# Kernel tuning notes

Measured on AMD Instinct MI355X. Metric: run time of the kernel, lower is better.

## Reference

```python
import jax, jax.numpy as jnp
import numpy as np

# Mamba2 defaults (mamba-ssm): expand=2, d_state=128, d_conv=4, headdim=64, ngroups=1
D_MODEL = 1024
D_INNER = 2 * D_MODEL            # 2048
D_STATE = 128
D_CONV = 4
HEADDIM = 64
NHEADS = D_INNER // HEADDIM      # 32
CONV_DIM = D_INNER + 2 * D_STATE # 2304 (x, B, C go through conv)
D_IN_PROJ = 2 * D_INNER + 2 * D_STATE + NHEADS  # 4384 (z, xBC, dt)
LN_EPS = 1e-6


def setup_inputs() -> dict:
    key = jax.random.key(0)
    ks = jax.random.split(key, 12)
    B, L, D = 8, 1024, D_MODEL
    x = jax.random.normal(ks[0], (B, L, D), jnp.float32)
    t = jax.random.normal(ks[1], (B, D), jnp.float32)
    y = jax.random.normal(ks[2], (B, L, D), jnp.float32)
    # adaLN linear (zero-init in the module; use small random values for a non-trivial baseline)
    w_ada = jax.random.normal(ks[3], (D, 3 * D), jnp.float32) * 0.02
    b_ada = jax.random.normal(ks[4], (3 * D,), jnp.float32) * 0.02
    # Mamba2 params
    w_in = jax.random.normal(ks[5], (D, D_IN_PROJ), jnp.float32) * (D ** -0.5)
    conv_w = jax.random.normal(ks[6], (CONV_DIM, D_CONV), jnp.float32) * (D_CONV ** -0.5)
    conv_b = jnp.zeros((CONV_DIM,), jnp.float32)
    # dt_bias = softplus^{-1}(dt) with dt log-uniform in [1e-3, 1e-1]
    dt0 = jnp.exp(jax.random.uniform(ks[7], (NHEADS,)) * (np.log(0.1) - np.log(0.001)) + np.log(0.001))
    dt_bias = dt0 + jnp.log(-jnp.expm1(-dt0))
    A_log = jnp.log(jax.random.uniform(ks[8], (NHEADS,), minval=1.0, maxval=16.0))
    D_param = jnp.ones((NHEADS,), jnp.float32)
    w_out = jax.random.normal(ks[9], (D_INNER, D), jnp.float32) * (D_INNER ** -0.5)
    return {"x": x, "t": t, "y": y, "w_ada": w_ada, "b_ada": b_ada, "w_in": w_in,
            "conv_w": conv_w, "conv_b": conv_b, "dt_bias": dt_bias, "A_log": A_log,
            "D_param": D_param, "w_out": w_out}


def _layernorm(x):
    mu = jnp.mean(x, axis=-1, keepdims=True)
    var = jnp.mean(jnp.square(x - mu), axis=-1, keepdims=True)
    return (x - mu) / jnp.sqrt(var + LN_EPS)


def _mamba2(u, w_in, conv_w, conv_b, dt_bias, A_log, D_param, w_out):
    B, L, _ = u.shape
    zxbcdt = u @ w_in  # [B, L, D_IN_PROJ]
    z = zxbcdt[..., :D_INNER]
    xBC = zxbcdt[..., D_INNER:D_INNER + CONV_DIM]
    dt = zxbcdt[..., D_INNER + CONV_DIM:]
    # depthwise causal conv1d (kernel=4) + silu
    xp = jnp.pad(xBC, ((0, 0), (D_CONV - 1, 0), (0, 0)))
    conv = conv_b
    for k in range(D_CONV):
        conv = conv + conv_w[:, k] * xp[:, k:k + L, :]
    xBC = jax.nn.silu(conv)
    xh = xBC[..., :D_INNER].reshape(B, L, NHEADS, HEADDIM)
    Bm = xBC[..., D_INNER:D_INNER + D_STATE]  # [B, L, N] (ngroups=1)
    Cm = xBC[..., D_INNER + D_STATE:]         # [B, L, N]
    dt = jax.nn.softplus(dt + dt_bias)        # [B, L, H]
    A = -jnp.exp(A_log)                       # [H]
    dA = jnp.exp(dt * A)                      # [B, L, H]
    dtx = dt[..., None] * xh                  # [B, L, H, P]

    def step(h, inp):
        dA_t, dtx_t, B_t, C_t = inp
        # h: [B, H, P, N]
        h = h * dA_t[:, :, None, None] + dtx_t[..., None] * B_t[:, None, None, :]
        y_t = jnp.einsum('bhpn,bn->bhp', h, C_t)
        return h, y_t

    h0 = jnp.zeros((B, NHEADS, HEADDIM, D_STATE), u.dtype)
    xs = (jnp.moveaxis(dA, 1, 0), jnp.moveaxis(dtx, 1, 0),
          jnp.moveaxis(Bm, 1, 0), jnp.moveaxis(Cm, 1, 0))
    _, ys = jax.lax.scan(step, h0, xs)        # ys: [L, B, H, P]
    yv = jnp.moveaxis(ys, 0, 1) + D_param[None, None, :, None] * xh
    yv = yv.reshape(B, L, D_INNER) * jax.nn.silu(z)  # rmsnorm=False -> silu(z) gating
    return yv @ w_out


def reference(x, t, y, w_ada, b_ada, w_in, conv_w, conv_b, dt_bias, A_log, D_param, w_out):
    at = jax.nn.silu(t) @ w_ada + b_ada   # [B, 3D]
    ay = jax.nn.silu(y) @ w_ada + b_ada   # [B, L, 3D]
    sh_t, sc_t, g_t = jnp.split(at, 3, axis=1)
    sh_y, sc_y, g_y = jnp.split(ay, 3, axis=2)
    shift = sh_t[:, None, :] + sh_y
    scale = sc_t[:, None, :] + sc_y
    gate = g_t[:, None, :] + g_y
    mod = _layernorm(x) * (1 + scale) + shift
    return gate * _mamba2(mod, w_in, conv_w, conv_b, dt_bias, A_log, D_param, w_out) + x
```

## Files before the change

kernel.cpp:

```cpp
#include <hip/hip_runtime.h>

typedef float f32x4 __attribute__((ext_vector_type(4)));
typedef __bf16 bf16x8 __attribute__((ext_vector_type(8)));
typedef unsigned short ushort;
typedef ushort ushort8 __attribute__((ext_vector_type(8)));
typedef ushort ushort4v __attribute__((ext_vector_type(4)));

#define DM 1024
#define DI 2048
#define DSTATE 128
#define NH 32
#define HD 64
#define CONVDIM 2304
#define DPROJ 4384
#define ROWS 8192

__device__ __forceinline__ float bf2f(ushort u){
  union { unsigned int i; float f; } v; v.i = ((unsigned int)u)<<16; return v.f;
}
__device__ __forceinline__ ushort f2bf(float f){
  union { float f; unsigned int i; } v; v.f = f;
  unsigned int r = v.i + 0x7FFFu + ((v.i>>16)&1u);
  return (ushort)(r>>16);
}
__device__ __forceinline__ float siluf(float x){ return x / (1.f + __expf(-x)); }

__device__ __forceinline__ void gload16(const ushort* g, ushort* l){
  __builtin_amdgcn_global_load_lds(
      (const __attribute__((address_space(1))) void*)g,
      (__attribute__((address_space(3))) void*)l, 16, 0, 0);
}

__global__ __launch_bounds__(256) void k_silu_cast(const float* __restrict__ in,
                                                   ushort* __restrict__ out, int n){
  int i = (blockIdx.x*256 + threadIdx.x)*4;
  if (i >= n) return;
  float4 v = *(const float4*)(in + i);
  ushort4v o;
  o.x = f2bf(siluf(v.x)); o.y = f2bf(siluf(v.y));
  o.z = f2bf(siluf(v.z)); o.w = f2bf(siluf(v.w));
  *(ushort4v*)(out + i) = o;
}

__global__ __launch_bounds__(256) void k_transpose_cast(const float* __restrict__ in,
                                                        ushort* __restrict__ out,
                                                        int K, int N){
  __shared__ float tile[32][33];
  int n0 = blockIdx.x*32, k0 = blockIdx.y*32;
  int tx = threadIdx.x & 31, ty = threadIdx.x >> 5;
  for (int r = ty; r < 32; r += 8) tile[r][tx] = in[(size_t)(k0+r)*N + n0+tx];
  __syncthreads();
  for (int r = ty; r < 32; r += 8) out[(size_t)(n0+r)*K + k0+tx] = f2bf(tile[tx][r]);
}

__global__ __launch_bounds__(256) void k_at(const float* __restrict__ t,
                                            const float* __restrict__ w_ada,
                                            const float* __restrict__ b_ada,
                                            float* __restrict__ at){
  __shared__ float st[1024];
  int b = blockIdx.y;
  int col = blockIdx.x*256 + threadIdx.x;
  for (int i = threadIdx.x; i < 1024; i += 256) st[i] = siluf(t[b*1024 + i]);
  __syncthreads();
  float acc = 0.f;
  for (int k = 0; k < 1024; ++k) acc += st[k] * w_ada[(size_t)k*3072 + col];
  at[b*3072 + col] = acc + b_ada[col];
}

#define STG(Q, KT) do{ \
  gload16(pA0 + (size_t)(KT)*32, &sm[(Q)*12288 + (wave*2+0)*512]); \
  gload16(pA1 + (size_t)(KT)*32, &sm[(Q)*12288 + (wave*2+1)*512]); \
  gload16(pB0 + (size_t)(KT)*32, &sm[(Q)*12288 + 8192 + wave*512]); }while(0)

#define CMP(BOFF) do{ \
  bf16x8 af[4], bfr[4]; \
  _Pragma("unroll") \
  for (int m=0;m<4;m++) af[m]  = *(const bf16x8*)&sm[(BOFF) + (wr*64 + m*16 + l16)*32 + kbs]; \
  _Pragma("unroll") \
  for (int n=0;n<4;n++) bfr[n] = *(const bf16x8*)&sm[(BOFF) + 8192 + (wc*64 + n*16 + l16)*32 + kbs]; \
  __builtin_amdgcn_s_setprio(1); \
  _Pragma("unroll") \
  for (int m=0;m<4;m++) \
    _Pragma("unroll") \
    for (int n=0;n<4;n++) \
      acc[m][n] = __builtin_amdgcn_mfma_f32_16x16x32_bf16(af[m], bfr[n], acc[m][n], 0, 0, 0); \
  __builtin_amdgcn_s_setprio(0); }while(0)

#define BODY(Q, T) do{ \
  STG(((Q)+2)%3, (T)+2); \
  CMP((Q)*12288); \
  asm volatile("s_waitcnt vmcnt(3)" ::: "memory"); \
  __builtin_amdgcn_s_barrier(); \
  __builtin_amdgcn_sched_barrier(0); }while(0)

template<int EPI>
__global__ __launch_bounds__(512)
void k_gemm(const ushort* __restrict__ Ag, const ushort* __restrict__ Bt,
            ushort* __restrict__ Cb, ushort* __restrict__ Cb2, ushort* __restrict__ Cb3,
            float* __restrict__ Cf,
            int M, int N, int K, int nbn,
            const float* __restrict__ bias, const float* __restrict__ at,
            const ushort* __restrict__ gateM, const float* __restrict__ xres){
  __shared__ __align__(16) ushort sm[3*12288];
  const int tid  = threadIdx.x;
  const int wave = tid >> 6, lane = tid & 63;
  const int nwg = gridDim.x, bid0 = blockIdx.x;
  const int wg = (bid0 & 7)*(nwg >> 3) + (bid0 >> 3);
  const int pg = nbn << 2;
  const int g  = wg / pg;
  const int rem = wg - g*pg;
  const int bm = (g << 2) + (rem & 3);
  const int bn = rem >> 2;
  const int wr = wave >> 1, wc = wave & 1;
  const int l16 = lane & 15, kb = lane >> 4;
  const int arow0 = (wave*2+0)*16 + (lane>>2);
  const int arow1 = (wave*2+1)*16 + (lane>>2);
  const int brow  = wave*16 + (lane>>2);
  const int kcs = (lane & 3) ^ ((lane>>3)&3);
  const int kbs = (kb ^ ((l16>>1)&3))*8;

  const ushort* pA0 = Ag + (size_t)(bm*256 + arow0)*K + kcs*8;
  const ushort* pA1 = Ag + (size_t)(bm*256 + arow1)*K + kcs*8;
  int br0 = bn*128 + brow; if (br0 > N-1) br0 = N-1;
  const ushort* pB0 = Bt + (size_t)br0*K + kcs*8;

  f32x4 acc[4][4];
#pragma unroll
  for (int m=0;m<4;m++)
#pragma unroll
    for (int n=0;n<4;n++) acc[m][n] = (f32x4){0.f,0.f,0.f,0.f};

  const int NT = K >> 5;
  const int NB = NT - 2;

  STG(0, 0); STG(1, 1);
  asm volatile("s_waitcnt vmcnt(3)" ::: "memory");
  __builtin_amdgcn_s_barrier();
  __builtin_amdgcn_sched_barrier(0);

  int T = 0;
  for (; T + 3 <= NB; T += 3){
    BODY(0, T); BODY(1, T+1); BODY(2, T+2);
  }
  if (NB - T >= 1) BODY(0, T);
  if (NB - T >= 2) BODY(1, T+1);

  {
    const int qa = NB % 3, qb = (NB + 1) % 3;
    CMP(qa*12288);
    asm volatile("s_waitcnt vmcnt(0)" ::: "memory");
    __builtin_amdgcn_s_barrier();
    __builtin_amdgcn_sched_barrier(0);
    CMP(qb*12288);
  }

#pragma unroll
  for (int m=0;m<4;m++){
    int grow_base = bm*256 + wr*64 + m*16 + (lane>>4)*4;
#pragma unroll
    for (int n=0;n<4;n++){
      int gcol = bn*128 + wc*64 + n*16 + l16;
      if (EPI == 0){
        if (gcol < N){
#pragma unroll
          for (int r=0;r<4;r++){
            int row = grow_base + r;
            float v = acc[m][n][r];
            if (gcol < 2048)      Cb [(size_t)row*2048 + gcol] = f2bf(v);
            else if (gcol < 4352) Cb2[(size_t)row*2304 + (gcol-2048)] = f2bf(v);
            else                  Cb3[(size_t)row*32   + (gcol-4352)] = f2bf(v);
          }
        }
      } else if (EPI == 1){
        float bv = bias[gcol];
#pragma unroll
        for (int r=0;r<4;r++){
          int row = grow_base + r;
          float v = acc[m][n][r] + bv + at[(row>>10)*3072 + gcol];
          if (gcol < 2048) Cb [(size_t)row*2048 + gcol] = f2bf(v);
          else             Cb2[(size_t)row*1024 + (gcol - 2048)] = f2bf(v);
        }
      } else {
#pragma unroll
        for (int r=0;r<4;r++){
          int row = grow_base + r;
          float g2 = bf2f(gateM[(size_t)row*1024 + gcol]);
          Cf[(size_t)row*1024 + gcol] = g2*acc[m][n][r] + xres[(size_t)row*1024 + gcol];
        }
      }
    }
  }
}

__global__ __launch_bounds__(256) void k_lnmod(const float* __restrict__ x,
                                               const ushort* __restrict__ Mss,
                                               ushort* __restrict__ mod){
  int row = blockIdx.x;
  const float* xr = x + (size_t)row*1024;
  float v[4]; float s = 0.f, s2 = 0.f;
#pragma unroll
  for (int j=0;j<4;j++){ v[j] = xr[threadIdx.x + j*256]; s += v[j]; s2 += v[j]*v[j]; }
#pragma unroll
  for (int o=32;o>0;o>>=1){ s += __shfl_down(s,o); s2 += __shfl_down(s2,o); }
  __shared__ float ls[4], ls2[4];
  int wv = threadIdx.x >> 6;
  if ((threadIdx.x & 63) == 0){ ls[wv] = s; ls2[wv] = s2; }
  __syncthreads();
  s  = ls[0]+ls[1]+ls[2]+ls[3];
  s2 = ls2[0]+ls2[1]+ls2[2]+ls2[3];
  float mu = s * (1.f/1024.f);
  float var = s2 * (1.f/1024.f) - mu*mu;
  float rstd = rsqrtf(var + 1e-6f);
  const ushort* Mr = Mss + (size_t)row*2048;
#pragma unroll
  for (int j=0;j<4;j++){
    int d = threadIdx.x + j*256;
    float sc = bf2f(Mr[1024 + d]);
    float sh = bf2f(Mr[d]);
    mod[(size_t)row*1024 + d] = f2bf((v[j]-mu)*rstd*(1.f+sc) + sh);
  }
}

__global__ __launch_bounds__(256) void k_convT(const ushort* __restrict__ xbc,
                                               const float* __restrict__ conv_w,
                                               const float* __restrict__ conv_b,
                                               ushort* __restrict__ co,
                                               ushort* __restrict__ xhT,
                                               ushort* __restrict__ BTg){
  __shared__ ushort lin[67*64];
  __shared__ __align__(16) ushort outb[64*76];
  const int cb = blockIdx.x, lb = blockIdx.y, b = blockIdx.z;
  const int ch0 = cb*64, l0 = lb*64;
  const int tid = threadIdx.x;
  for (int q = tid; q < 67*8; q += 256){
    int r = q >> 3, c8 = q & 7;
    int l = l0 - 3 + r;
    ushort8 v = {0,0,0,0,0,0,0,0};
    if (l >= 0) v = *(const ushort8*)(xbc + (size_t)(b*1024 + l)*CONVDIM + ch0 + c8*8);
    *(ushort8*)&lin[r*64 + c8*8] = v;
  }
  __syncthreads();
  const int ch = tid & 63, lg = tid >> 6;
  const int chg = ch0 + ch;
  const float w0 = conv_w[chg*4+0], w1 = conv_w[chg*4+1];
  const float w2 = conv_w[chg*4+2], w3 = conv_w[chg*4+3];
  const float cbv = conv_b[chg];
  __align__(16) ushort o[16];
#pragma unroll
  for (int j = 0; j < 16; ++j){
    int r = lg*16 + j;
    float a = cbv + w0*bf2f(lin[r*64+ch])     + w1*bf2f(lin[(r+1)*64+ch])
                  + w2*bf2f(lin[(r+2)*64+ch]) + w3*bf2f(lin[(r+3)*64+ch]);
    o[j] = f2bf(siluf(a));
  }
  if (cb < 34){
    *(ushort8*)&outb[ch*76 + lg*16]     = *(ushort8*)&o[0];
    *(ushort8*)&outb[ch*76 + lg*16 + 8] = *(ushort8*)&o[8];
    __syncthreads();
    int row = tid >> 2, seg = tid & 3;
    ushort8 v0 = *(ushort8*)&outb[row*76 + seg*16];
    ushort8 v1 = *(ushort8*)&outb[row*76 + seg*16 + 8];
    ushort* dst = (cb < 32)
      ? (xhT + (size_t)(b*2048 + ch0 + row)*1024 + l0 + seg*16)
      : (BTg + (size_t)(b*128 + (ch0 - 2048) + row)*1024 + l0 + seg*16);
    *(ushort8*)dst = v0; *(ushort8*)(dst+8) = v1;
  }
  if (cb >= 32){
    __syncthreads();
#pragma unroll
    for (int j = 0; j < 16; ++j) outb[(lg*16+j)*76 + ch] = o[j];
    __syncthreads();
    int l = tid >> 2, seg = tid & 3;
    ushort8 v0 = *(ushort8*)&outb[l*76 + seg*16];
    ushort8 v1 = *(ushort8*)&outb[l*76 + seg*16 + 8];
    ushort* dst = co + (size_t)(b*1024 + l0 + l)*CONVDIM + ch0 + seg*16;
    *(ushort8*)dst = v0; *(ushort8*)(dst+8) = v1;
  }
}

__global__ __launch_bounds__(256) void k_chunkstate(
    const ushort* __restrict__ xhT, const ushort* __restrict__ BTg,
    const ushort* __restrict__ dtc,
    const float* __restrict__ dt_bias, const float* __restrict__ A_log,
    ushort* __restrict__ Sc, float* __restrict__ Dcb){
  __shared__ __align__(16) ushort sXG[64*128];
  __shared__ __align__(16) ushort sBT[128*128];
  __shared__ float sG[128];
  const int bid = blockIdx.x;
  const int h = bid & 31, bc = bid >> 5, b = bc >> 3, c = bc & 7;
  const int tid = threadIdx.x, wave = tid >> 6, lane = tid & 63;
  const int l16 = lane & 15, l4 = lane >> 4;
  const int sci = (b*32 + h)*8 + c;
  {
    const ushort* src = BTg + (size_t)(b*128)*1024 + c*128;
    for (int i2 = 0; i2 < 8; ++i2){
      int itg = wave*8 + i2;
      int r = itg*4 + l4;
      int cc = l16 ^ (r & 7);
      gload16(src + (size_t)r*1024 + cc*8, &sBT[itg*512]);
    }
  }
  const float Ah = -__expf(A_log[h]);
  if (wave == 0){
    const int row0 = b*1024 + c*128;
    float bi = dt_bias[h];
    float d0 = bf2f(dtc[(size_t)(row0 + 2*lane    )*32 + h]) + bi;
    float d1 = bf2f(dtc[(size_t)(row0 + 2*lane + 1)*32 + h]) + bi;
    d0 = (d0 > 20.f) ? d0 : log1pf(__expf(d0));
    d1 = (d1 > 20.f) ? d1 : log1pf(__expf(d1));
    float p = d0 + d1;
#pragma unroll
    for (int o = 1; o < 64; o <<= 1){
      float tp = __shfl_up(p, o);
      if (lane >= o) p += tp;
    }
    float cs127 = __shfl(p, 63);
    sG[2*lane    ] = __expf(Ah*(cs127 - (p - d1))) * d0;
    sG[2*lane + 1] = __expf(Ah*(cs127 - p)) * d1;
    if (lane == 0) Dcb[sci] = __expf(Ah*cs127);
  }
  __syncthreads();
  {
    const ushort* xsrc = xhT + (size_t)(b*2048 + h*64)*1024 + c*128;
    for (int q = tid; q < 1024; q += 256){
      int r = q >> 4, cc = q & 15;
      ushort8 v = *(const ushort8*)(xsrc + (size_t)r*1024 + cc*8);
      ushort8 o;
#pragma unroll
      for (int j = 0; j < 8; ++j) o[j] = f2bf(bf2f(v[j]) * sG[cc*8 + j]);
      *(ushort8*)&sXG[r*128 + ((cc ^ (r & 7))*8)] = o;
    }
  }
  __syncthreads();
  f32x4 acc[4][2];
#pragma unroll
  for (int m=0;m<4;m++)
#pragma unroll
    for (int nf=0;nf<2;nf++) acc[m][nf] = (f32x4){0.f,0.f,0.f,0.f};
  for (int ks = 0; ks < 4; ++ks){
    bf16x8 av[4], bv[2];
#pragma unroll
    for (int m = 0; m < 4; ++m){
      int rp = m*16 + l16;
      av[m] = *(const bf16x8*)&sXG[rp*128 + (((ks*4 + l4) ^ (rp & 7))*8)];
    }
#pragma unroll
    for (int nf = 0; nf < 2; ++nf){
      int rn = wave*32 + nf*16 + l16;
      bv[nf] = *(const bf16x8*)&sBT[rn*128 + (((ks*4 + l4) ^ (rn & 7))*8)];
    }
#pragma unroll
    for (int m = 0; m < 4; ++m)
#pragma unroll
      for (int nf = 0; nf < 2; ++nf)
        acc[m][nf] = __builtin_amdgcn_mfma_f32_16x16x32_bf16(av[m], bv[nf], acc[m][nf], 0, 0, 0);
  }
  const size_t base = (size_t)sci * 8192;
#pragma unroll
  for (int m = 0; m < 4; ++m)
#pragma unroll
    for (int nf = 0; nf < 2; ++nf)
#pragma unroll
      for (int r = 0; r < 4; ++r){
        int p = m*16 + l4*4 + r;
        int n = wave*32 + nf*16 + l16;
        Sc[base + p*128 + n] = f2bf(acc[m][nf][r]);
      }
}

__global__ __launch_bounds__(256) void k_chunkscan(ushort* __restrict__ Sc,
                                                   const float* __restrict__ Dcb){
  size_t idx = (size_t)blockIdx.x*256 + threadIdx.x;
  int bh = (int)(idx >> 13);
  int pn = (int)(idx & 8191);
  float hv = 0.f;
  for (int c = 0; c < 8; ++c){
    size_t o = (size_t)(bh*8 + c)*8192 + pn;
    float s = bf2f(Sc[o]);
    float dc = Dcb[bh*8 + c];
    Sc[o] = f2bf(hv);
    hv = hv*dc + s;
  }
}

__global__ __launch_bounds__(256, 2) void k_ssd(
    const ushort* __restrict__ co, const ushort* __restrict__ zz,
    const ushort* __restrict__ dtc, const ushort* __restrict__ xhT,
    const ushort* __restrict__ Hin,
    const float* __restrict__ dt_bias, const float* __restrict__ A_log,
    const float* __restrict__ D_param,
    ushort* __restrict__ yv){
  __shared__ __align__(16) ushort sC [128*128];
  __shared__ __align__(16) ushort sBP[128*128];
  __shared__ float csv[128], dtv[128];
  const int bid = blockIdx.x;
  const int h = bid & 31, bc = bid >> 5, b = bc >> 3, c = bc & 7;
  const int tid = threadIdx.x, wave = tid >> 6, lane = tid & 63;
  const int l16 = lane & 15, l4 = lane >> 4;
  const int wr = wave >> 1, wc = wave & 1;
  const int row0 = b*1024 + c*128;
  const ushort* cbase = co + (size_t)row0*CONVDIM;
  for (int i2 = 0; i2 < 8; ++i2){
    int itg = wave*8 + i2;
    int r = itg*4 + l4;
    int cc = l16 ^ (r & 7);
    gload16(cbase + (size_t)r*CONVDIM + 2176 + cc*8, &sC [itg*512]);
    gload16(cbase + (size_t)r*CONVDIM + 2048 + cc*8, &sBP[itg*512]);
  }
  bf16x8 xbr[2][4], hbr[2][4];
  {
    const size_t hbase = (size_t)((b*32 + h)*8 + c)*8192;
#pragma unroll
    for (int n = 0; n < 2; ++n){
      const int rp = wc*32 + n*16 + l16;
      const ushort* xrow = xhT + (size_t)(b*2048 + h*64 + rp)*1024 + c*128;
      const ushort* hrow = Hin + hbase + (size_t)rp*128;
#pragma unroll
      for (int ks = 0; ks < 4; ++ks){
        xbr[n][ks] = *(const bf16x8*)(xrow + (ks*4 + l4)*8);
        hbr[n][ks] = *(const bf16x8*)(hrow + (ks*4 + l4)*8);
      }
    }
  }
  const float Ah = -__expf(A_log[h]);
  if (wave == 0){
    float bi = dt_bias[h];
    float d0 = bf2f(dtc[(size_t)(row0 + 2*lane    )*32 + h]) + bi;
    float d1 = bf2f(dtc[(size_t)(row0 + 2*lane + 1)*32 + h]) + bi;
    d0 = (d0 > 20.f) ? d0 : log1pf(__expf(d0));
    d1 = (d1 > 20.f) ? d1 : log1pf(__expf(d1));
    float p = d0 + d1;
#pragma unroll
    for (int o = 1; o < 64; o <<= 1){
      float tp = __shfl_up(p, o);
      if (lane >= o) p += tp;
    }
    csv[2*lane    ] = p - d1;
    csv[2*lane + 1] = p;
    dtv[2*lane    ] = d0;
    dtv[2*lane + 1] = d1;
  }
  __syncthreads();
  f32x4 acc[4][4];
#pragma unroll
  for (int m=0;m<4;m++)
#pragma unroll
    for (int n=0;n<4;n++) acc[m][n] = (f32x4){0.f,0.f,0.f,0.f};
  for (int ks = 0; ks < 4; ++ks){
    bf16x8 av[4], bv[4];
#pragma unroll
    for (int m = 0; m < 4; ++m){
      int ri = wr*64 + m*16 + l16;
      av[m] = *(const bf16x8*)&sC[ri*128 + (((ks*4 + l4) ^ (ri & 7))*8)];
    }
#pragma unroll
    for (int n = 0; n < 4; ++n){
      int rs = wc*64 + n*16 + l16;
      bv[n] = *(const bf16x8*)&sBP[rs*128 + (((ks*4 + l4) ^ (rs & 7))*8)];
    }
#pragma unroll
    for (int m = 0; m < 4; ++m)
#pragma unroll
      for (int n = 0; n < 4; ++n)
        acc[m][n] = __builtin_amdgcn_mfma_f32_16x16x32_bf16(av[m], bv[n], acc[m][n], 0, 0, 0);
  }
  __syncthreads();
  const float Dp = D_param[h];
#pragma unroll
  for (int m = 0; m < 4; ++m){
#pragma unroll
    for (int r = 0; r < 4; ++r){
      int i = wr*64 + m*16 + l4*4 + r;
      float ci = csv[i];
#pragma unroll
      for (int n = 0; n < 4; ++n){
        int s = wc*64 + n*16 + l16;
        float e = __expf(Ah*(ci - csv[s]));
        float v = (i >= s) ? acc[m][n][r]*e*dtv[s] : 0.f;
        if (i == s) v += Dp;
        sBP[i*128 + (s ^ ((i & 7)<<3))] = f2bf(v);
      }
    }
  }
  __syncthreads();
  f32x4 accY[4][2], accI[4][2];
#pragma unroll
  for (int m=0;m<4;m++)
#pragma unroll
    for (int n=0;n<2;n++){ accY[m][n] = (f32x4){0.f,0.f,0.f,0.f}; accI[m][n] = (f32x4){0.f,0.f,0.f,0.f}; }
#pragma unroll
  for (int ks = 0; ks < 4; ++ks){
    bf16x8 pa[4], ca[4];
#pragma unroll
    for (int m = 0; m < 4; ++m){
      int ri = wr*64 + m*16 + l16;
      int off = ((ks*4 + l4) ^ (ri & 7))*8;
      pa[m] = *(const bf16x8*)&sBP[ri*128 + off];
      ca[m] = *(const bf16x8*)&sC [ri*128 + off];
    }
#pragma unroll
    for (int m = 0; m < 4; ++m)
#pragma unroll
      for (int n = 0; n < 2; ++n){
        accY[m][n] = __builtin_amdgcn_mfma_f32_16x16x32_bf16(pa[m], xbr[n][ks], accY[m][n], 0, 0, 0);
        accI[m][n] = __builtin_amdgcn_mfma_f32_16x16x32_bf16(ca[m], hbr[n][ks], accI[m][n], 0, 0, 0);
      }
  }
#pragma unroll
  for (int m = 0; m < 4; ++m){
#pragma unroll
    for (int r = 0; r < 4; ++r){
      int i = wr*64 + m*16 + l4*4 + r;
      float Ei = __expf(Ah*csv[i]);
      int grow = row0 + i;
#pragma unroll
      for (int n = 0; n < 2; ++n){
        int p = wc*32 + n*16 + l16;
        float yvl = accY[m][n][r] + Ei*accI[m][n][r];
        float z = bf2f(zz[(size_t)grow*2048 + h*64 + p]);
        yv[(size_t)grow*DI + h*64 + p] = f2bf(yvl * siluf(z));
      }
    }
  }
}

extern "C" void kernel_launch(void* const* d_in, const int* in_sizes, int n_in,
                              void* d_out, int out_size, void* d_ws, size_t ws_size,
                              hipStream_t stream){
  const float* x       = (const float*)d_in[0];
  const float* t       = (const float*)d_in[1];
  const float* y       = (const float*)d_in[2];
  const float* w_ada   = (const float*)d_in[3];
  const float* b_ada   = (const float*)d_in[4];
  const float* w_in    = (const float*)d_in[5];
  const float* conv_w  = (const float*)d_in[6];
  const float* conv_b  = (const float*)d_in[7];
  const float* dt_bias = (const float*)d_in[8];
  const float* A_log   = (const float*)d_in[9];
  const float* D_param = (const float*)d_in[10];
  const float* w_out   = (const float*)d_in[11];

  char* w = (char*)d_ws;
  size_t off = 0;
  auto alloc = [&](size_t bytes)->char*{
    char* p = w + off; off += (bytes + 255) & ~(size_t)255; return p;
  };
  ushort* zz    = (ushort*)alloc((size_t)ROWS*2048*2);
  ushort* xbc   = (ushort*)alloc((size_t)ROWS*CONVDIM*2);
  ushort* dtc   = (ushort*)alloc((size_t)ROWS*32*2);
  ushort* co    = (ushort*)alloc((size_t)ROWS*CONVDIM*2);
  ushort* Mss   = (ushort*)alloc((size_t)ROWS*2048*2);
  ushort* Mg    = (ushort*)alloc((size_t)ROWS*1024*2);
  ushort* yv    = (ushort*)alloc((size_t)ROWS*DI*2);
  ushort* woutT = (ushort*)alloc(1024ull*2048*2);
  ushort* waT   = (ushort*)alloc(3072ull*1024*2);
  ushort* winT  = (ushort*)alloc(4608ull*1024*2);
  float*  atb   = (float*) alloc(8ull*3072*4);
  ushort* Ya    = (ushort*)alloc((size_t)ROWS*1024*2);
  ushort* BTg   = (ushort*)alloc((size_t)8*128*1024*2);
  float*  Dcb   = (float*) alloc(2048ull*4);
  ushort* xhT   = Mss;
  ushort* Sc    = xbc;

  k_silu_cast<<<dim3(ROWS*1024/(256*4)), 256, 0, stream>>>(y, Ya, ROWS*1024);
  k_transpose_cast<<<dim3(96,32),  256, 0, stream>>>(w_ada, waT,  1024, 3072);
  k_transpose_cast<<<dim3(137,32), 256, 0, stream>>>(w_in,  winT, 1024, 4384);
  k_transpose_cast<<<dim3(32,64),  256, 0, stream>>>(w_out, woutT, 2048, 1024);
  k_at<<<dim3(12,8), 256, 0, stream>>>(t, w_ada, b_ada, atb);
  k_gemm<1><<<dim3(768), 512, 0, stream>>>(Ya, waT, Mss, Mg, nullptr, nullptr, ROWS, 3072, 1024, 24,
                                           b_ada, atb, nullptr, nullptr);
  k_lnmod<<<dim3(ROWS), 256, 0, stream>>>(x, Mss, Ya);
  k_gemm<0><<<dim3(1120), 512, 0, stream>>>(Ya, winT, zz, xbc, dtc, nullptr, ROWS, DPROJ, 1024, 35,
                                            nullptr, nullptr, nullptr, nullptr);
  k_convT<<<dim3(36,16,8), 256, 0, stream>>>(xbc, conv_w, conv_b, co, xhT, BTg);
  k_chunkstate<<<dim3(2048), 256, 0, stream>>>(xhT, BTg, dtc, dt_bias, A_log, Sc, Dcb);
  k_chunkscan<<<dim3(8192), 256, 0, stream>>>(Sc, Dcb);
  k_ssd<<<dim3(2048), 256, 0, stream>>>(co, zz, dtc, xhT, Sc, dt_bias, A_log, D_param, yv);
  k_gemm<2><<<dim3(256), 512, 0, stream>>>(yv, woutT, nullptr, nullptr, nullptr, (float*)d_out,
                                           ROWS, 1024, 2048, 8, nullptr, nullptr, Mg, x);
}
```

Measured before the change: 421.4 us.

## Fuse chunk-state and inter-chunk scan into one sequential-chunk kernel; compact B/C buffer

Merges the chunk-state GEMM and the inter-chunk recurrence into a single kernel. Each block owns a (batch, head, p-half, n-half) tile and walks the 8 chunks in order, keeping the running state in MFMA accumulators and writing the per-chunk initial state directly. This removes the separate scan kernel and the write-then-reread of per-chunk states and decay factors. The conv output now stores only the B/C channels in a compact 256-wide buffer, which cuts write traffic and gives k_ssd contiguous reads. In exchange, the scan kernel launches fewer blocks (1024), and its chunks run serially inside each block with a barrier per chunk, so latency is harder to hide.

```diff
diff --git a/kernel.cpp b/kernel.cpp
--- a/kernel.cpp
+++ b/kernel.cpp
@@ -224,7 +224,7 @@
 __global__ __launch_bounds__(256) void k_convT(const ushort* __restrict__ xbc,
                                                const float* __restrict__ conv_w,
                                                const float* __restrict__ conv_b,
-                                               ushort* __restrict__ co,
+                                               ushort* __restrict__ BC,
                                                ushort* __restrict__ xhT,
                                                ushort* __restrict__ BTg){
   __shared__ ushort lin[67*64];
@@ -273,118 +273,110 @@
     int l = tid >> 2, seg = tid & 3;
     ushort8 v0 = *(ushort8*)&outb[l*76 + seg*16];
     ushort8 v1 = *(ushort8*)&outb[l*76 + seg*16 + 8];
-    ushort* dst = co + (size_t)(b*1024 + l0 + l)*CONVDIM + ch0 + seg*16;
+    ushort* dst = BC + (size_t)(b*1024 + l0 + l)*256 + (ch0 - 2048) + seg*16;
     *(ushort8*)dst = v0; *(ushort8*)(dst+8) = v1;
   }
 }
 
-__global__ __launch_bounds__(256) void k_chunkstate(
+__global__ __launch_bounds__(256) void k_chscan(
     const ushort* __restrict__ xhT, const ushort* __restrict__ BTg,
     const ushort* __restrict__ dtc,
     const float* __restrict__ dt_bias, const float* __restrict__ A_log,
-    ushort* __restrict__ Sc, float* __restrict__ Dcb){
-  __shared__ __align__(16) ushort sXG[64*128];
-  __shared__ __align__(16) ushort sBT[128*128];
+    ushort* __restrict__ Hin){
+  __shared__ __align__(16) ushort sX[32*128];
+  __shared__ __align__(16) ushort sB[64*128];
   __shared__ float sG[128];
+  __shared__ float sDc;
   const int bid = blockIdx.x;
-  const int h = bid & 31, bc = bid >> 5, b = bc >> 3, c = bc & 7;
+  const int nh = bid & 1, ph = (bid >> 1) & 1, h = (bid >> 2) & 31, b = bid >> 7;
   const int tid = threadIdx.x, wave = tid >> 6, lane = tid & 63;
   const int l16 = lane & 15, l4 = lane >> 4;
-  const int sci = (b*32 + h)*8 + c;
-  {
-    const ushort* src = BTg + (size_t)(b*128)*1024 + c*128;
-    for (int i2 = 0; i2 < 8; ++i2){
-      int itg = wave*8 + i2;
-      int r = itg*4 + l4;
-      int cc = l16 ^ (r & 7);
-      gload16(src + (size_t)r*1024 + cc*8, &sBT[itg*512]);
-    }
-  }
   const float Ah = -__expf(A_log[h]);
-  if (wave == 0){
-    const int row0 = b*1024 + c*128;
-    float bi = dt_bias[h];
-    float d0 = bf2f(dtc[(size_t)(row0 + 2*lane    )*32 + h]) + bi;
-    float d1 = bf2f(dtc[(size_t)(row0 + 2*lane + 1)*32 + h]) + bi;
-    d0 = (d0 > 20.f) ? d0 : log1pf(__expf(d0));
-    d1 = (d1 > 20.f) ? d1 : log1pf(__expf(d1));
-    float p = d0 + d1;
-#pragma unroll
-    for (int o = 1; o < 64; o <<= 1){
-      float tp = __shfl_up(p, o);
-      if (lane >= o) p += tp;
-    }
-    float cs127 = __shfl(p, 63);
-    sG[2*lane    ] = __expf(Ah*(cs127 - (p - d1))) * d0;
-    sG[2*lane + 1] = __expf(Ah*(cs127 - p)) * d1;
-    if (lane == 0) Dcb[sci] = __expf(Ah*cs127);
-  }
-  __syncthreads();
-  {
-    const ushort* xsrc = xhT + (size_t)(b*2048 + h*64)*1024 + c*128;
-    for (int q = tid; q < 1024; q += 256){
-      int r = q >> 4, cc = q & 15;
-      ushort8 v = *(const ushort8*)(xsrc + (size_t)r*1024 + cc*8);
-      ushort8 o;
-#pragma unroll
-      for (int j = 0; j < 8; ++j) o[j] = f2bf(bf2f(v[j]) * sG[cc*8 + j]);
-      *(ushort8*)&sXG[r*128 + ((cc ^ (r & 7))*8)] = o;
-    }
-  }
-  __syncthreads();
-  f32x4 acc[4][2];
-#pragma unroll
-  for (int m=0;m<4;m++)
-#pragma unroll
-    for (int nf=0;nf<2;nf++) acc[m][nf] = (f32x4){0.f,0.f,0.f,0.f};
-  for (int ks = 0; ks < 4; ++ks){
-    bf16x8 av[4], bv[2];
-#pragma unroll
-    for (int m = 0; m < 4; ++m){
-      int rp = m*16 + l16;
-      av[m] = *(const bf16x8*)&sXG[rp*128 + (((ks*4 + l4) ^ (rp & 7))*8)];
-    }
-#pragma unroll
-    for (int nf = 0; nf < 2; ++nf){
-      int rn = wave*32 + nf*16 + l16;
-      bv[nf] = *(const bf16x8*)&sBT[rn*128 + (((ks*4 + l4) ^ (rn & 7))*8)];
-    }
-#pragma unroll
-    for (int m = 0; m < 4; ++m)
-#pragma unroll
-      for (int nf = 0; nf < 2; ++nf)
-        acc[m][nf] = __builtin_amdgcn_mfma_f32_16x16x32_bf16(av[m], bv[nf], acc[m][nf], 0, 0, 0);
-  }
-  const size_t base = (size_t)sci * 8192;
-#pragma unroll
-  for (int m = 0; m < 4; ++m)
-#pragma unroll
-    for (int nf = 0; nf < 2; ++nf)
-#pragma unroll
-      for (int r = 0; r < 4; ++r){
-        int p = m*16 + l4*4 + r;
-        int n = wave*32 + nf*16 + l16;
-        Sc[base + p*128 + n] = f2bf(acc[m][nf][r]);
-      }
-}
-
-__global__ __launch_bounds__(256) void k_chunkscan(ushort* __restrict__ Sc,
-                                                   const float* __restrict__ Dcb){
-  size_t idx = (size_t)blockIdx.x*256 + threadIdx.x;
-  int bh = (int)(idx >> 13);
-  int pn = (int)(idx & 8191);
-  float hv = 0.f;
+  const size_t hinBase0 = (size_t)((b*32 + h)*8)*8192;
+
+  f32x4 acc[2];
+  acc[0] = (f32x4){0.f,0.f,0.f,0.f};
+  acc[1] = (f32x4){0.f,0.f,0.f,0.f};
+
   for (int c = 0; c < 8; ++c){
-    size_t o = (size_t)(bh*8 + c)*8192 + pn;
-    float s = bf2f(Sc[o]);
-    float dc = Dcb[bh*8 + c];
-    Sc[o] = f2bf(hv);
-    hv = hv*dc + s;
+    {
+      const ushort* src = BTg + (size_t)(b*128 + nh*64)*1024 + c*128;
+#pragma unroll
+      for (int i2 = 0; i2 < 4; ++i2){
+        int itg = wave*4 + i2;
+        int r = itg*4 + l4;
+        int cc = l16 ^ (r & 7);
+        gload16(src + (size_t)r*1024 + cc*8, &sB[itg*512]);
+      }
+    }
+    if (wave == 0){
+      const int row0 = b*1024 + c*128;
+      float bi = dt_bias[h];
+      float d0 = bf2f(dtc[(size_t)(row0 + 2*lane    )*32 + h]) + bi;
+      float d1 = bf2f(dtc[(size_t)(row0 + 2*lane + 1)*32 + h]) + bi;
+      d0 = (d0 > 20.f) ? d0 : log1pf(__expf(d0));
+      d1 = (d1 > 20.f) ? d1 : log1pf(__expf(d1));
+      float p = d0 + d1;
+#pragma unroll
+      for (int o = 1; o < 64; o <<= 1){
+        float tp = __shfl_up(p, o);
+        if (lane >= o) p += tp;
+      }
+      float cs127 = __shfl(p, 63);
+      sG[2*lane    ] = __expf(Ah*(cs127 - (p - d1))) * d0;
+      sG[2*lane + 1] = __expf(Ah*(cs127 - p)) * d1;
+      if (lane == 0) sDc = __expf(Ah*cs127);
+    }
+    __syncthreads();
+    float dcv = sDc;
+    {
+      size_t base = hinBase0 + (size_t)c*8192;
+#pragma unroll
+      for (int m = 0; m < 2; ++m)
+#pragma unroll
+        for (int r = 0; r < 4; ++r){
+          int p = ph*32 + m*16 + l4*4 + r;
+          int n = nh*64 + wave*16 + l16;
+          Hin[base + p*128 + n] = f2bf(acc[m][r]);
+        }
+    }
+    {
+      const ushort* xsrc = xhT + (size_t)(b*2048 + h*64 + ph*32)*1024 + c*128;
+#pragma unroll
+      for (int q0 = 0; q0 < 2; ++q0){
+        int q = tid + q0*256;
+        int r = q >> 4, cc = q & 15;
+        ushort8 v = *(const ushort8*)(xsrc + (size_t)r*1024 + cc*8);
+        ushort8 o;
+#pragma unroll
+        for (int j = 0; j < 8; ++j) o[j] = f2bf(bf2f(v[j]) * sG[cc*8 + j]);
+        *(ushort8*)&sX[r*128 + ((cc ^ (r & 7))*8)] = o;
+      }
+    }
+    asm volatile("s_waitcnt vmcnt(0)" ::: "memory");
+    __syncthreads();
+    acc[0] = acc[0]*dcv;
+    acc[1] = acc[1]*dcv;
+#pragma unroll
+    for (int ks = 0; ks < 4; ++ks){
+      bf16x8 av[2], bv;
+#pragma unroll
+      for (int m = 0; m < 2; ++m){
+        int rp = m*16 + l16;
+        av[m] = *(const bf16x8*)&sX[rp*128 + (((ks*4 + l4) ^ (rp & 7))*8)];
+      }
+      int rn = wave*16 + l16;
+      bv = *(const bf16x8*)&sB[rn*128 + (((ks*4 + l4) ^ (rn & 7))*8)];
+#pragma unroll
+      for (int m = 0; m < 2; ++m)
+        acc[m] = __builtin_amdgcn_mfma_f32_16x16x32_bf16(av[m], bv, acc[m], 0, 0, 0);
+    }
+    __syncthreads();
   }
 }
 
 __global__ __launch_bounds__(256, 2) void k_ssd(
-    const ushort* __restrict__ co, const ushort* __restrict__ zz,
+    const ushort* __restrict__ BC, const ushort* __restrict__ zz,
     const ushort* __restrict__ dtc, const ushort* __restrict__ xhT,
     const ushort* __restrict__ Hin,
     const float* __restrict__ dt_bias, const float* __restrict__ A_log,
@@ -399,13 +391,13 @@
   const int l16 = lane & 15, l4 = lane >> 4;
   const int wr = wave >> 1, wc = wave & 1;
   const int row0 = b*1024 + c*128;
-  const ushort* cbase = co + (size_t)row0*CONVDIM;
+  const ushort* cbase = BC + (size_t)row0*256;
   for (int i2 = 0; i2 < 8; ++i2){
     int itg = wave*8 + i2;
     int r = itg*4 + l4;
     int cc = l16 ^ (r & 7);
-    gload16(cbase + (size_t)r*CONVDIM + 2176 + cc*8, &sC [itg*512]);
-    gload16(cbase + (size_t)r*CONVDIM + 2048 + cc*8, &sBP[itg*512]);
+    gload16(cbase + (size_t)r*256 + 128 + cc*8, &sC [itg*512]);
+    gload16(cbase + (size_t)r*256 +       cc*8, &sBP[itg*512]);
   }
   bf16x8 xbr[2][4], hbr[2][4];
   {
@@ -548,7 +540,7 @@
   ushort* zz    = (ushort*)alloc((size_t)ROWS*2048*2);
   ushort* xbc   = (ushort*)alloc((size_t)ROWS*CONVDIM*2);
   ushort* dtc   = (ushort*)alloc((size_t)ROWS*32*2);
-  ushort* co    = (ushort*)alloc((size_t)ROWS*CONVDIM*2);
+  ushort* BCb   = (ushort*)alloc((size_t)ROWS*256*2);
   ushort* Mss   = (ushort*)alloc((size_t)ROWS*2048*2);
   ushort* Mg    = (ushort*)alloc((size_t)ROWS*1024*2);
   ushort* yv    = (ushort*)alloc((size_t)ROWS*DI*2);
@@ -558,9 +550,8 @@
   float*  atb   = (float*) alloc(8ull*3072*4);
   ushort* Ya    = (ushort*)alloc((size_t)ROWS*1024*2);
   ushort* BTg   = (ushort*)alloc((size_t)8*128*1024*2);
-  float*  Dcb   = (float*) alloc(2048ull*4);
   ushort* xhT   = Mss;
-  ushort* Sc    = xbc;
+  ushort* Hin   = xbc;
 
   k_silu_cast<<<dim3(ROWS*1024/(256*4)), 256, 0, stream>>>(y, Ya, ROWS*1024);
   k_transpose_cast<<<dim3(96,32),  256, 0, stream>>>(w_ada, waT,  1024, 3072);
@@ -572,10 +563,9 @@
   k_lnmod<<<dim3(ROWS), 256, 0, stream>>>(x, Mss, Ya);
   k_gemm<0><<<dim3(1120), 512, 0, stream>>>(Ya, winT, zz, xbc, dtc, nullptr, ROWS, DPROJ, 1024, 35,
                                             nullptr, nullptr, nullptr, nullptr);
-  k_convT<<<dim3(36,16,8), 256, 0, stream>>>(xbc, conv_w, conv_b, co, xhT, BTg);
-  k_chunkstate<<<dim3(2048), 256, 0, stream>>>(xhT, BTg, dtc, dt_bias, A_log, Sc, Dcb);
-  k_chunkscan<<<dim3(8192), 256, 0, stream>>>(Sc, Dcb);
-  k_ssd<<<dim3(2048), 256, 0, stream>>>(co, zz, dtc, xhT, Sc, dt_bias, A_log, D_param, yv);
+  k_convT<<<dim3(36,16,8), 256, 0, stream>>>(xbc, conv_w, conv_b, BCb, xhT, BTg);
+  k_chscan<<<dim3(1024), 256, 0, stream>>>(xhT, BTg, dtc, dt_bias, A_log, Hin);
+  k_ssd<<<dim3(2048), 256, 0, stream>>>(BCb, zz, dtc, xhT, Hin, dt_bias, A_log, D_param, yv);
   k_gemm<2><<<dim3(256), 512, 0, stream>>>(yv, woutT, nullptr, nullptr, nullptr, (float*)d_out,
                                            ROWS, 1024, 2048, 8, nullptr, nullptr, Mg, x);
 }
```

Result: no change. 416.9 us (-1.1%).
